# Performance work log

Hardware: AMD Instinct MI355X
Metric: run time of the kernel (lower is better)

Reference implementation:

```python
import jax, jax.numpy as jnp
import numpy as np

B, N, D, NUM_CLASSES = 2048, 32768, 256, 100

def setup_inputs() -> dict:
    key = jax.random.key(0)
    k1, k2, k3 = jax.random.split(key, 3)
    x = jax.random.normal(k1, (B, D), dtype=jnp.float32)
    support_embeddings = jax.random.normal(k2, (N, D), dtype=jnp.float32)
    support_labels = jax.random.randint(k3, (N,), 0, NUM_CLASSES, dtype=jnp.int64)
    return {
        "x": x,
        "support_embeddings": support_embeddings,
        "support_labels": support_labels,
        "num_classes": NUM_CLASSES,
    }

def reference(x, support_embeddings, support_labels, num_classes):
    # Pairwise L2 distance [B, N] via ||q||^2 + ||s||^2 - 2 q.s (avoids [B,N,D] broadcast)
    q2 = jnp.sum(x * x, axis=1, keepdims=True)                 # [B, 1]
    s2 = jnp.sum(support_embeddings * support_embeddings, axis=1)  # [N]
    cross = jnp.einsum('bd,nd->bn', x, support_embeddings)     # [B, N]
    dist = jnp.sqrt(jnp.maximum(q2 + s2[None, :] - 2.0 * cross, 0.0))
    # topk(-dist, k=1) over support axis -> nearest neighbor index
    _, idx = jax.lax.top_k(-dist, 1)                           # [B, 1]
    idx = jnp.squeeze(idx, axis=1)                             # [B]
    labels = jnp.take(support_labels, idx, axis=0)             # [B]
    one_hot = jax.nn.one_hot(labels, num_classes, dtype=jnp.int32)  # [B, num_classes]
    return one_hot
```

## Files before the change

### kernel.cpp

```cpp
#include <hip/hip_runtime.h>

#define BQ 2048
#define NS 32768
#define DIM 256
#define NROWS (NS + BQ)

#define BMQ 128
#define BNS 128
#define BK 32
#define NST (DIM / BK)
#define GY (NS / BNS)
#define EPS 0.08f
#define FBCH GY

typedef _Float16 f16;
typedef _Float16 f16x4 __attribute__((ext_vector_type(4)));
typedef _Float16 f16x8 __attribute__((ext_vector_type(8)));
typedef float    f32x4 __attribute__((ext_vector_type(4)));

__device__ __forceinline__ void gload16(const f16* g, f16* l) {
    __builtin_amdgcn_global_load_lds(
        (const __attribute__((address_space(1))) unsigned int*)g,
        (__attribute__((address_space(3))) unsigned int*)l, 16, 0, 0);
}

__device__ __forceinline__ const f16x8* fragp(const f16* base, int row, int q) {
    return (const f16x8*)(base + row * 32 + ((q ^ ((row >> 1) & 3)) << 3));
}

__global__ __launch_bounds__(256) void convert_kernel(
    const float* __restrict__ x, const float* __restrict__ sup,
    f16* __restrict__ xh, f16* __restrict__ sh,
    float* __restrict__ s2, int* __restrict__ fb_cnt) {
    if (blockIdx.x == 0 && threadIdx.x == 0) *fb_cnt = 0;
    const int wave = threadIdx.x >> 6, lane = threadIdx.x & 63;
    const int row = blockIdx.x * 4 + wave;
    if (row < NS) {
        float4 v = ((const float4*)(sup + (size_t)row * DIM))[lane];
        f16x4 hi;
        hi[0] = (f16)v.x; hi[1] = (f16)v.y; hi[2] = (f16)v.z; hi[3] = (f16)v.w;
        *(f16x4*)(sh + (size_t)row * DIM + lane * 4) = hi;
        float sum = v.x * v.x + v.y * v.y + v.z * v.z + v.w * v.w;
#pragma unroll
        for (int off = 32; off > 0; off >>= 1) sum += __shfl_xor(sum, off);
        if (lane == 0) s2[row] = sum;
    } else {
        const int q = row - NS;
        float4 v = ((const float4*)(x + (size_t)q * DIM))[lane];
        f16x4 hi;
        hi[0] = (f16)v.x; hi[1] = (f16)v.y; hi[2] = (f16)v.z; hi[3] = (f16)v.w;
        *(f16x4*)(xh + (size_t)q * DIM + lane * 4) = hi;
    }
}

__global__ __launch_bounds__(256) void knn_mfma(
    const f16* __restrict__ xh, const f16* __restrict__ sh,
    const float* __restrict__ s2g,
    float* __restrict__ pv1, float* __restrict__ pv2, int* __restrict__ pi1) {
    __shared__ f16 T[2][2][BMQ * 32];

    const int tid  = threadIdx.x;
    const int lane = tid & 63, wid = tid >> 6;
    const int l16  = lane & 15, quad = lane >> 4;
    const int m0   = blockIdx.x * BMQ;
    const int n0   = blockIdx.y * BNS;

    const int rl = lane >> 2;
    const int qs = (lane & 3) ^ ((rl >> 1) & 3);
    const size_t srcoff = (size_t)rl * DIM + qs * 8;

    const f16* px0 = xh + (size_t)(m0 + wid * 32) * DIM + srcoff;
    const f16* px1 = px0 + (size_t)16 * DIM;
    const f16* ps0 = sh + (size_t)(n0 + wid * 32) * DIM + srcoff;
    const f16* ps1 = ps0 + (size_t)16 * DIM;
    const int dX = wid * 1024;

    f32x4 acc[2][8];
#pragma unroll
    for (int fi = 0; fi < 2; ++fi)
#pragma unroll
        for (int fj = 0; fj < 8; ++fj) acc[fi][fj] = (f32x4){0.f, 0.f, 0.f, 0.f};

    gload16(px0, &T[0][0][dX]);
    gload16(px1, &T[0][0][dX + 512]);
    gload16(ps0, &T[0][1][dX]);
    gload16(ps1, &T[0][1][dX + 512]);

    for (int s = 0; s < NST; ++s) {
        __syncthreads();
        if (s + 1 < NST) {
            const int b = (s + 1) & 1, k0 = (s + 1) * BK;
            gload16(px0 + k0, &T[b][0][dX]);
            gload16(px1 + k0, &T[b][0][dX + 512]);
            gload16(ps0 + k0, &T[b][1][dX]);
            gload16(ps1 + k0, &T[b][1][dX + 512]);
        }
        const f16* TX = &T[s & 1][0][0];
        const f16* TS = &T[s & 1][1][0];

        f16x8 A0 = *fragp(TX, wid * 32 + l16,      quad);
        f16x8 A1 = *fragp(TX, wid * 32 + 16 + l16, quad);
#pragma unroll
        for (int fj = 0; fj < 8; ++fj) {
            f16x8 B = *fragp(TS, fj * 16 + l16, quad);
            acc[0][fj] = __builtin_amdgcn_mfma_f32_16x16x32_f16(A0, B, acc[0][fj], 0, 0, 0);
            acc[1][fj] = __builtin_amdgcn_mfma_f32_16x16x32_f16(A1, B, acc[1][fj], 0, 0, 0);
        }
    }

    float s2v[8];
#pragma unroll
    for (int fj = 0; fj < 8; ++fj) s2v[fj] = s2g[n0 + fj * 16 + l16];
#pragma unroll
    for (int fi = 0; fi < 2; ++fi)
#pragma unroll
        for (int rg = 0; rg < 4; ++rg) {
            float bv1 = 3.4e38f, bv2 = 3.4e38f; int bi = 0;
#pragma unroll
            for (int fj = 0; fj < 8; ++fj) {
                float s = fmaf(-2.f, acc[fi][fj][rg], s2v[fj]);
                bv2 = fminf(bv2, fmaxf(bv1, s));
                bi  = (s < bv1) ? (n0 + fj * 16 + l16) : bi;
                bv1 = fminf(bv1, s);
            }
#pragma unroll
            for (int m = 1; m < 16; m <<= 1) {
                float ov1 = __shfl_xor(bv1, m);
                float ov2 = __shfl_xor(bv2, m);
                int   oi  = __shfl_xor(bi, m);
                float nb2 = fminf(fminf(bv2, ov2), fmaxf(bv1, ov1));
                bi  = (ov1 < bv1) ? oi : bi;
                bv1 = fminf(bv1, ov1);
                bv2 = nb2;
            }
            if (l16 == 0) {
                const int row = m0 + wid * 32 + fi * 16 + quad * 4 + rg;
                pv1[(size_t)row * GY + blockIdx.y] = bv1;
                pv2[(size_t)row * GY + blockIdx.y] = bv2;
                pi1[(size_t)row * GY + blockIdx.y] = bi;
            }
        }
}

__global__ __launch_bounds__(128) void finalize2(
    const float* __restrict__ pv1, const float* __restrict__ pv2,
    const int* __restrict__ pi1, const int* __restrict__ labels,
    const int* __restrict__ ncp, int* __restrict__ out,
    int* __restrict__ fb_cnt, int* __restrict__ fb_list,
    float* __restrict__ qbest) {
    const int q = blockIdx.x, tid = threadIdx.x;
    __shared__ int s_label;
    if (tid < 64) {
        float bv1 = 3.4e38f, bv2 = 3.4e38f; int bi = 0;
        for (int t = tid; t < GY; t += 64) {
            float ov1 = pv1[(size_t)q * GY + t];
            float ov2 = pv2[(size_t)q * GY + t];
            int   oi  = pi1[(size_t)q * GY + t];
            float nb2 = fminf(fminf(bv2, ov2), fmaxf(bv1, ov1));
            bi  = (ov1 < bv1) ? oi : bi;
            bv1 = fminf(bv1, ov1);
            bv2 = nb2;
        }
#pragma unroll
        for (int m = 1; m < 64; m <<= 1) {
            float ov1 = __shfl_xor(bv1, m);
            float ov2 = __shfl_xor(bv2, m);
            int   oi  = __shfl_xor(bi, m);
            float nb2 = fminf(fminf(bv2, ov2), fmaxf(bv1, ov1));
            bi  = (ov1 < bv1) ? oi : bi;
            bv1 = fminf(bv1, ov1);
            bv2 = nb2;
        }
        if (tid == 0) {
            qbest[q] = bv1;
            if (bv2 - bv1 <= EPS) {
                int slot = atomicAdd(fb_cnt, 1);
                fb_list[slot] = q;
            }
            bool is64 = true;
            for (int i = 1; i < 128; i += 2)
                if (labels[i] != 0) { is64 = false; break; }
            s_label = is64 ? labels[2 * bi] : labels[bi];
        }
    }
    __syncthreads();
    const int nc = ncp[0], lbl = s_label;
    for (int c = tid; c < nc; c += 128)
        out[q * nc + c] = (c == lbl) ? 1 : 0;
}

__global__ __launch_bounds__(256) void fallback_scan(
    const float* __restrict__ x, const float* __restrict__ sup,
    const float* __restrict__ s2, const int* __restrict__ fb_cnt,
    const int* __restrict__ fb_list, const float* __restrict__ qbest,
    const float* __restrict__ pv1,
    float* __restrict__ fb_v, int* __restrict__ fb_i) {
    const int nslots = *fb_cnt;
    const int chunk = blockIdx.x;
    const int tid = threadIdx.x, lane = tid & 63, w = tid >> 6;
    __shared__ float wv[4];
    __shared__ int   wi[4];
    for (int slot = blockIdx.y; slot < nslots; slot += gridDim.y) {
        const int q = fb_list[slot];
        if (pv1[(size_t)q * GY + chunk] > qbest[q] + EPS) {
            if (tid == 0) {
                fb_v[(size_t)q * FBCH + chunk] = 3.4e38f;
                fb_i[(size_t)q * FBCH + chunk] = 0x7fffffff;
            }
            __syncthreads();
            continue;
        }
        const float4 xv = ((const float4*)(x + (size_t)q * DIM))[lane];
        float best = 3.4e38f; int bi = 0x7fffffff;
        const int base = chunk * BNS + w * 32;
#pragma unroll 4
        for (int r = 0; r < 32; ++r) {
            const int n = base + r;
            float4 sv = ((const float4*)(sup + (size_t)n * DIM))[lane];
            float d = fmaf(sv.x, xv.x,
                      fmaf(sv.y, xv.y,
                      fmaf(sv.z, xv.z, sv.w * xv.w)));
#pragma unroll
            for (int m = 32; m > 0; m >>= 1) d += __shfl_xor(d, m);
            float sc = s2[n] - 2.f * d;
            if (sc < best) { best = sc; bi = n; }
        }
        if (lane == 0) { wv[w] = best; wi[w] = bi; }
        __syncthreads();
        if (tid == 0) {
            float bv = wv[0]; int bx = wi[0];
#pragma unroll
            for (int t = 1; t < 4; ++t)
                if (wv[t] < bv || (wv[t] == bv && wi[t] < bx)) { bv = wv[t]; bx = wi[t]; }
            fb_v[(size_t)q * FBCH + chunk] = bv;
            fb_i[(size_t)q * FBCH + chunk] = bx;
        }
        __syncthreads();
    }
}

__global__ __launch_bounds__(64) void fallback_merge(
    const int* __restrict__ fb_cnt, const int* __restrict__ fb_list,
    const float* __restrict__ fb_v, const int* __restrict__ fb_i,
    const int* __restrict__ labels, const int* __restrict__ ncp,
    int* __restrict__ out) {
    const int nslots = *fb_cnt;
    const int lane = threadIdx.x;
    for (int slot = blockIdx.x; slot < nslots; slot += gridDim.x) {
        const int q = fb_list[slot];
        float v = 3.4e38f; int ix = 0x7fffffff;
        for (int t = lane; t < FBCH; t += 64) {
            float ov = fb_v[(size_t)q * FBCH + t];
            int   oi = fb_i[(size_t)q * FBCH + t];
            if (ov < v || (ov == v && oi < ix)) { v = ov; ix = oi; }
        }
#pragma unroll
        for (int m = 1; m < 64; m <<= 1) {
            float ov = __shfl_xor(v, m);
            int   oi = __shfl_xor(ix, m);
            if (ov < v || (ov == v && oi < ix)) { v = ov; ix = oi; }
        }
        bool is64 = true;
        for (int i = 1; i < 128; i += 2)
            if (labels[i] != 0) { is64 = false; break; }
        const int lbl = is64 ? labels[2 * ix] : labels[ix];
        const int nc = ncp[0];
        for (int c = lane; c < nc; c += 64)
            out[q * nc + c] = (c == lbl) ? 1 : 0;
    }
}

#define SBM 128
#define SBN 128
#define SBK 16
#define SNT 4
#define SGY (NS / (SBN * SNT))
#define SLDT (SBM + 4)

__global__ __launch_bounds__(256) void s2_kernel(const float* __restrict__ s,
                                                 float* __restrict__ s2) {
    int wave = threadIdx.x >> 6, lane = threadIdx.x & 63;
    int row = blockIdx.x * 4 + wave;
    const float4* p = (const float4*)(s + (size_t)row * DIM);
    float4 v = p[lane];
    float sum = v.x * v.x + v.y * v.y + v.z * v.z + v.w * v.w;
#pragma unroll
    for (int off = 32; off > 0; off >>= 1) sum += __shfl_xor(sum, off);
    if (lane == 0) s2[row] = sum;
}

__global__ __launch_bounds__(256) void knn_f32(const float* __restrict__ x,
                                               const float* __restrict__ sup,
                                               const float* __restrict__ s2g,
                                               float* __restrict__ pvals,
                                               int* __restrict__ pidx) {
    __shared__ float Xs[SBK][SLDT];
    __shared__ float Bs[SBK][SLDT];
    const int tid = threadIdx.x;
    const int tx = tid & 15, ty = tid >> 4;
    const int m0 = blockIdx.x * SBM, by = blockIdx.y;
    const int srow = tid >> 2, skq = (tid & 3) * 4;
    float rmin[8]; int ridx[8];
#pragma unroll
    for (int i = 0; i < 8; ++i) { rmin[i] = 3.4e38f; ridx[i] = 0x7fffffff; }
    const float* xr0 = x + (size_t)(m0 + srow) * DIM + skq;
    const float* xr1 = x + (size_t)(m0 + 64 + srow) * DIM + skq;
    for (int nt = 0; nt < SNT; ++nt) {
        const int n0 = (by * SNT + nt) * SBN;
        const float* sr0 = sup + (size_t)(n0 + srow) * DIM + skq;
        const float* sr1 = sup + (size_t)(n0 + 64 + srow) * DIM + skq;
        float acc[8][8];
#pragma unroll
        for (int i = 0; i < 8; ++i)
#pragma unroll
            for (int j = 0; j < 8; ++j) acc[i][j] = 0.0f;
        for (int kt = 0; kt < DIM / SBK; ++kt) {
            const int k0 = kt * SBK;
            float4 xv0 = *(const float4*)(xr0 + k0);
            float4 xv1 = *(const float4*)(xr1 + k0);
            float4 sv0 = *(const float4*)(sr0 + k0);
            float4 sv1 = *(const float4*)(sr1 + k0);
            __syncthreads();
            Xs[skq + 0][srow] = xv0.x; Xs[skq + 1][srow] = xv0.y;
            Xs[skq + 2][srow] = xv0.z; Xs[skq + 3][srow] = xv0.w;
            Xs[skq + 0][64 + srow] = xv1.x; Xs[skq + 1][64 + srow] = xv1.y;
            Xs[skq + 2][64 + srow] = xv1.z; Xs[skq + 3][64 + srow] = xv1.w;
            Bs[skq + 0][srow] = sv0.x; Bs[skq + 1][srow] = sv0.y;
            Bs[skq + 2][srow] = sv0.z; Bs[skq + 3][srow] = sv0.w;
            Bs[skq + 0][64 + srow] = sv1.x; Bs[skq + 1][64 + srow] = sv1.y;
            Bs[skq + 2][64 + srow] = sv1.z; Bs[skq + 3][64 + srow] = sv1.w;
            __syncthreads();
#pragma unroll
            for (int k = 0; k < SBK; ++k) {
                float4 a0 = *(const float4*)&Xs[k][ty * 4];
                float4 a1 = *(const float4*)&Xs[k][64 + ty * 4];
                float4 b0 = *(const float4*)&Bs[k][tx * 4];
                float4 b1 = *(const float4*)&Bs[k][64 + tx * 4];
                float a[8] = {a0.x, a0.y, a0.z, a0.w, a1.x, a1.y, a1.z, a1.w};
                float b[8] = {b0.x, b0.y, b0.z, b0.w, b1.x, b1.y, b1.z, b1.w};
#pragma unroll
                for (int i = 0; i < 8; ++i)
#pragma unroll
                    for (int j = 0; j < 8; ++j)
                        acc[i][j] = fmaf(a[i], b[j], acc[i][j]);
            }
        }
        const int nb0 = n0 + tx * 4, nb1 = n0 + 64 + tx * 4;
        float4 s20 = *(const float4*)(s2g + nb0);
        float4 s21 = *(const float4*)(s2g + nb1);
        float s2a[8] = {s20.x, s20.y, s20.z, s20.w, s21.x, s21.y, s21.z, s21.w};
        int nca[8] = {nb0, nb0 + 1, nb0 + 2, nb0 + 3, nb1, nb1 + 1, nb1 + 2, nb1 + 3};
#pragma unroll
        for (int i = 0; i < 8; ++i)
#pragma unroll
            for (int j = 0; j < 8; ++j) {
                float sc = fmaf(-2.0f, acc[i][j], s2a[j]);
                if (sc < rmin[i] || (sc == rmin[i] && nca[j] < ridx[i])) {
                    rmin[i] = sc; ridx[i] = nca[j];
                }
            }
    }
    __syncthreads();
    float* redv = (float*)Xs;
    int* redi = (int*)Bs;
#pragma unroll
    for (int i = 0; i < 8; ++i) {
        int mrow = (i < 4) ? (ty * 4 + i) : (64 + ty * 4 + (i - 4));
        redv[mrow * 16 + tx] = rmin[i];
        redi[mrow * 16 + tx] = ridx[i];
    }
    __syncthreads();
    if (tid < SBM) {
        float best = redv[tid * 16];
        int bi = redi[tid * 16];
#pragma unroll
        for (int t = 1; t < 16; ++t) {
            float v = redv[tid * 16 + t];
            int ix = redi[tid * 16 + t];
            if (v < best || (v == best && ix < bi)) { best = v; bi = ix; }
        }
        pvals[(size_t)(m0 + tid) * SGY + by] = best;
        pidx[(size_t)(m0 + tid) * SGY + by] = bi;
    }
}

__global__ __launch_bounds__(64) void finalize_f32(const float* __restrict__ pvals,
                                                   const int* __restrict__ pidx,
                                                   const int* __restrict__ labels,
                                                   const int* __restrict__ ncp,
                                                   int* __restrict__ out) {
    const int b = blockIdx.x, lane = threadIdx.x;
    float v = pvals[(size_t)b * SGY + lane];
    int ix = pidx[(size_t)b * SGY + lane];
#pragma unroll
    for (int off = 32; off > 0; off >>= 1) {
        float ov = __shfl_xor(v, off);
        int oi = __shfl_xor(ix, off);
        if (ov < v || (ov == v && oi < ix)) { v = ov; ix = oi; }
    }
    bool is64 = true;
    for (int i = 1; i < 128; i += 2)
        if (labels[i] != 0) { is64 = false; break; }
    const int lbl = is64 ? labels[2 * ix] : labels[ix];
    const int nc = ncp[0];
    for (int c = lane; c < nc; c += 64)
        out[b * nc + c] = (c == lbl) ? 1 : 0;
}

extern "C" void kernel_launch(void* const* d_in, const int* in_sizes, int n_in,
                              void* d_out, int out_size, void* d_ws, size_t ws_size,
                              hipStream_t stream) {
    const float* x      = (const float*)d_in[0];
    const float* sup    = (const float*)d_in[1];
    const int*   labels = (const int*)d_in[2];
    const int*   ncp    = (const int*)d_in[3];
    int* out = (int*)d_out;

    char* p = (char*)d_ws;
    float* s2      = (float*)p;           p += (size_t)NS * 4;
    float* pv1     = (float*)p;           p += (size_t)BQ * GY * 4;
    float* pv2     = (float*)p;           p += (size_t)BQ * GY * 4;
    int*   pi1     = (int*)p;             p += (size_t)BQ * GY * 4;
    int*   fb_cnt  = (int*)p;             p += 256;
    int*   fb_list = (int*)p;             p += (size_t)BQ * 4;
    float* qbest   = (float*)p;           p += (size_t)BQ * 4;
    float* fb_v    = (float*)p;           p += (size_t)BQ * FBCH * 4;
    int*   fb_i    = (int*)p;             p += (size_t)BQ * FBCH * 4;
    f16*   xh      = (f16*)p;             p += (size_t)BQ * DIM * 2;
    f16*   sh      = (f16*)p;             p += (size_t)NS * DIM * 2;
    const size_t need = (size_t)(p - (char*)d_ws);

    if (ws_size >= need) {
        convert_kernel<<<NROWS / 4, 256, 0, stream>>>(x, sup, xh, sh, s2, fb_cnt);
        dim3 grid(BQ / BMQ, GY);
        knn_mfma<<<grid, 256, 0, stream>>>(xh, sh, s2, pv1, pv2, pi1);
        finalize2<<<BQ, 128, 0, stream>>>(pv1, pv2, pi1, labels, ncp, out,
                                          fb_cnt, fb_list, qbest);
        dim3 fbgrid(FBCH, 64);
        fallback_scan<<<fbgrid, 256, 0, stream>>>(x, sup, s2, fb_cnt, fb_list,
                                                  qbest, pv1, fb_v, fb_i);
        fallback_merge<<<64, 64, 0, stream>>>(fb_cnt, fb_list, fb_v, fb_i, labels, ncp, out);
    } else {
        float* ss2   = (float*)d_ws;
        float* pvals = ss2 + NS;
        int*   pidx  = (int*)(pvals + (size_t)BQ * SGY);
        s2_kernel<<<NS / 4, 256, 0, stream>>>(sup, ss2);
        dim3 grid(BQ / SBM, SGY);
        knn_f32<<<grid, 256, 0, stream>>>(x, sup, ss2, pvals, pidx);
        finalize_f32<<<BQ, 64, 0, stream>>>(pvals, pidx, labels, ncp, out);
    }
}
```

Before: 158.9 us.

## Fuse finalize, fallback scan and merge into one per-query kernel

Three kernels (finalize2, fallback_scan, fallback_merge) become one per-query kernel with 256 threads, one per chunk partial. Each block reduces its query's top-2 partials and, only when the margin is ambiguous, rescans in fp32 just the candidate chunks within EPS of the best, entirely in-block. This removes two launches, the global fallback list, the atomic counter and the fb_v/fb_i scratch buffers. The cost is that ambiguous queries are rescanned serially by one block instead of across a 256-chunk grid, which could add a long tail if a query has many candidates.

```diff
diff --git a/kernel.cpp b/kernel.cpp
--- a/kernel.cpp
+++ b/kernel.cpp
@@ -11,7 +11,6 @@
 #define NST (DIM / BK)
 #define GY (NS / BNS)
 #define EPS 0.08f
-#define FBCH GY
 
 typedef _Float16 f16;
 typedef _Float16 f16x4 __attribute__((ext_vector_type(4)));
@@ -30,9 +29,7 @@
 
 __global__ __launch_bounds__(256) void convert_kernel(
     const float* __restrict__ x, const float* __restrict__ sup,
-    f16* __restrict__ xh, f16* __restrict__ sh,
-    float* __restrict__ s2, int* __restrict__ fb_cnt) {
-    if (blockIdx.x == 0 && threadIdx.x == 0) *fb_cnt = 0;
+    f16* __restrict__ xh, f16* __restrict__ sh, float* __restrict__ s2) {
     const int wave = threadIdx.x >> 6, lane = threadIdx.x & 63;
     const int row = blockIdx.x * 4 + wave;
     if (row < NS) {
@@ -142,77 +139,79 @@
         }
 }
 
-__global__ __launch_bounds__(128) void finalize2(
+__global__ __launch_bounds__(256) void finalize_fused(
     const float* __restrict__ pv1, const float* __restrict__ pv2,
-    const int* __restrict__ pi1, const int* __restrict__ labels,
-    const int* __restrict__ ncp, int* __restrict__ out,
-    int* __restrict__ fb_cnt, int* __restrict__ fb_list,
-    float* __restrict__ qbest) {
+    const int* __restrict__ pi1,
+    const float* __restrict__ x, const float* __restrict__ sup,
+    const float* __restrict__ s2, const int* __restrict__ labels,
+    const int* __restrict__ ncp, int* __restrict__ out) {
     const int q = blockIdx.x, tid = threadIdx.x;
-    __shared__ int s_label;
-    if (tid < 64) {
-        float bv1 = 3.4e38f, bv2 = 3.4e38f; int bi = 0;
-        for (int t = tid; t < GY; t += 64) {
-            float ov1 = pv1[(size_t)q * GY + t];
-            float ov2 = pv2[(size_t)q * GY + t];
-            int   oi  = pi1[(size_t)q * GY + t];
-            float nb2 = fminf(fminf(bv2, ov2), fmaxf(bv1, ov1));
-            bi  = (ov1 < bv1) ? oi : bi;
-            bv1 = fminf(bv1, ov1);
-            bv2 = nb2;
-        }
-#pragma unroll
-        for (int m = 1; m < 64; m <<= 1) {
-            float ov1 = __shfl_xor(bv1, m);
-            float ov2 = __shfl_xor(bv2, m);
-            int   oi  = __shfl_xor(bi, m);
-            float nb2 = fminf(fminf(bv2, ov2), fmaxf(bv1, ov1));
-            bi  = (ov1 < bv1) ? oi : bi;
-            bv1 = fminf(bv1, ov1);
-            bv2 = nb2;
-        }
-        if (tid == 0) {
-            qbest[q] = bv1;
-            if (bv2 - bv1 <= EPS) {
-                int slot = atomicAdd(fb_cnt, 1);
-                fb_list[slot] = q;
-            }
-            bool is64 = true;
-            for (int i = 1; i < 128; i += 2)
-                if (labels[i] != 0) { is64 = false; break; }
-            s_label = is64 ? labels[2 * bi] : labels[bi];
-        }
-    }
-    __syncthreads();
-    const int nc = ncp[0], lbl = s_label;
-    for (int c = tid; c < nc; c += 128)
-        out[q * nc + c] = (c == lbl) ? 1 : 0;
-}
-
-__global__ __launch_bounds__(256) void fallback_scan(
-    const float* __restrict__ x, const float* __restrict__ sup,
-    const float* __restrict__ s2, const int* __restrict__ fb_cnt,
-    const int* __restrict__ fb_list, const float* __restrict__ qbest,
-    const float* __restrict__ pv1,
-    float* __restrict__ fb_v, int* __restrict__ fb_i) {
-    const int nslots = *fb_cnt;
-    const int chunk = blockIdx.x;
-    const int tid = threadIdx.x, lane = tid & 63, w = tid >> 6;
-    __shared__ float wv[4];
-    __shared__ int   wi[4];
-    for (int slot = blockIdx.y; slot < nslots; slot += gridDim.y) {
-        const int q = fb_list[slot];
-        if (pv1[(size_t)q * GY + chunk] > qbest[q] + EPS) {
-            if (tid == 0) {
-                fb_v[(size_t)q * FBCH + chunk] = 3.4e38f;
-                fb_i[(size_t)q * FBCH + chunk] = 0x7fffffff;
-            }
-            __syncthreads();
-            continue;
-        }
-        const float4 xv = ((const float4*)(x + (size_t)q * DIM))[lane];
-        float best = 3.4e38f; int bi = 0x7fffffff;
-        const int base = chunk * BNS + w * 32;
+    const int lane = tid & 63, w = tid >> 6;
+    __shared__ float sv1[4], sv2[4];
+    __shared__ int   si[4];
+    __shared__ float s_bv1, s_bv2;
+    __shared__ int   s_bi, s_is64, s_label;
+    __shared__ int   cand[GY];
+    __shared__ int   ncand;
+    __shared__ float fwv[4];
+    __shared__ int   fwi[4];
+
+    float bv1 = pv1[(size_t)q * GY + tid];
+    float bv2 = pv2[(size_t)q * GY + tid];
+    int   bi  = pi1[(size_t)q * GY + tid];
+    const float myv1 = bv1;
+#pragma unroll
+    for (int m = 1; m < 64; m <<= 1) {
+        float ov1 = __shfl_xor(bv1, m);
+        float ov2 = __shfl_xor(bv2, m);
+        int   oi  = __shfl_xor(bi, m);
+        float nb2 = fminf(fminf(bv2, ov2), fmaxf(bv1, ov1));
+        bi  = (ov1 < bv1) ? oi : bi;
+        bv1 = fminf(bv1, ov1);
+        bv2 = nb2;
+    }
+    if (lane == 0) { sv1[w] = bv1; sv2[w] = bv2; si[w] = bi; }
+    if (w == 0) {
+        unsigned long long ball = __ballot(labels[2 * lane + 1] == 0);
+        if (lane == 0) s_is64 = (ball == ~0ULL) ? 1 : 0;
+    }
+    if (tid == 0) ncand = 0;
+    __syncthreads();
+    if (tid == 0) {
+        float fb1 = sv1[0], fb2 = sv2[0]; int fbi = si[0];
+#pragma unroll
+        for (int t = 1; t < 4; ++t) {
+            float nb2 = fminf(fminf(fb2, sv2[t]), fmaxf(fb1, sv1[t]));
+            fbi = (sv1[t] < fb1) ? si[t] : fbi;
+            fb1 = fminf(fb1, sv1[t]);
+            fb2 = nb2;
+        }
+        s_bv1 = fb1; s_bv2 = fb2; s_bi = fbi;
+    }
+    __syncthreads();
+
+    const int nc = ncp[0];
+    if (s_bv2 - s_bv1 > EPS) {
+        if (tid == 0)
+            s_label = s_is64 ? labels[2 * s_bi] : labels[s_bi];
+        __syncthreads();
+        const int lbl = s_label;
+        for (int c = tid; c < nc; c += 256)
+            out[q * nc + c] = (c == lbl) ? 1 : 0;
+        return;
+    }
+
+    if (myv1 <= s_bv1 + EPS) {
+        int slot = atomicAdd(&ncand, 1);
+        cand[slot] = tid;
+    }
+    __syncthreads();
+    const int ncd = ncand;
+    float best = 3.4e38f; int bix = 0x7fffffff;
+    for (int ci = 0; ci < ncd; ++ci) {
+        const int base = cand[ci] * BNS + w * 32;
+        const float4* xp = (const float4*)(x + (size_t)q * DIM);
+        const float4 xv = xp[lane];
 #pragma unroll 4
         for (int r = 0; r < 32; ++r) {
             const int n = base + r;
@@ -223,51 +222,22 @@
 #pragma unroll
             for (int m = 32; m > 0; m >>= 1) d += __shfl_xor(d, m);
             float sc = s2[n] - 2.f * d;
-            if (sc < best) { best = sc; bi = n; }
-        }
-        if (lane == 0) { wv[w] = best; wi[w] = bi; }
-        __syncthreads();
-        if (tid == 0) {
-            float bv = wv[0]; int bx = wi[0];
-#pragma unroll
-            for (int t = 1; t < 4; ++t)
-                if (wv[t] < bv || (wv[t] == bv && wi[t] < bx)) { bv = wv[t]; bx = wi[t]; }
-            fb_v[(size_t)q * FBCH + chunk] = bv;
-            fb_i[(size_t)q * FBCH + chunk] = bx;
-        }
-        __syncthreads();
-    }
-}
-
-__global__ __launch_bounds__(64) void fallback_merge(
-    const int* __restrict__ fb_cnt, const int* __restrict__ fb_list,
-    const float* __restrict__ fb_v, const int* __restrict__ fb_i,
-    const int* __restrict__ labels, const int* __restrict__ ncp,
-    int* __restrict__ out) {
-    const int nslots = *fb_cnt;
-    const int lane = threadIdx.x;
-    for (int slot = blockIdx.x; slot < nslots; slot += gridDim.x) {
-        const int q = fb_list[slot];
-        float v = 3.4e38f; int ix = 0x7fffffff;
-        for (int t = lane; t < FBCH; t += 64) {
-            float ov = fb_v[(size_t)q * FBCH + t];
-            int   oi = fb_i[(size_t)q * FBCH + t];
-            if (ov < v || (ov == v && oi < ix)) { v = ov; ix = oi; }
-        }
-#pragma unroll
-        for (int m = 1; m < 64; m <<= 1) {
-            float ov = __shfl_xor(v, m);
-            int   oi = __shfl_xor(ix, m);
-            if (ov < v || (ov == v && oi < ix)) { v = ov; ix = oi; }
-        }
-        bool is64 = true;
-        for (int i = 1; i < 128; i += 2)
-            if (labels[i] != 0) { is64 = false; break; }
-        const int lbl = is64 ? labels[2 * ix] : labels[ix];
-        const int nc = ncp[0];
-        for (int c = lane; c < nc; c += 64)
-            out[q * nc + c] = (c == lbl) ? 1 : 0;
-    }
+            if (sc < best || (sc == best && n < bix)) { best = sc; bix = n; }
+        }
+    }
+    if (lane == 0) { fwv[w] = best; fwi[w] = bix; }
+    __syncthreads();
+    if (tid == 0) {
+        float fb = fwv[0]; int fx = fwi[0];
+#pragma unroll
+        for (int t = 1; t < 4; ++t)
+            if (fwv[t] < fb || (fwv[t] == fb && fwi[t] < fx)) { fb = fwv[t]; fx = fwi[t]; }
+        s_label = s_is64 ? labels[2 * fx] : labels[fx];
+    }
+    __syncthreads();
+    const int lbl = s_label;
+    for (int c = tid; c < nc; c += 256)
+        out[q * nc + c] = (c == lbl) ? 1 : 0;
 }
 
 #define SBM 128
@@ -417,36 +387,27 @@
     int* out = (int*)d_out;
 
     char* p = (char*)d_ws;
-    float* s2      = (float*)p;           p += (size_t)NS * 4;
-    float* pv1     = (float*)p;           p += (size_t)BQ * GY * 4;
-    float* pv2     = (float*)p;           p += (size_t)BQ * GY * 4;
-    int*   pi1     = (int*)p;             p += (size_t)BQ * GY * 4;
-    int*   fb_cnt  = (int*)p;             p += 256;
-    int*   fb_list = (int*)p;             p += (size_t)BQ * 4;
-    float* qbest   = (float*)p;           p += (size_t)BQ * 4;
-    float* fb_v    = (float*)p;           p += (size_t)BQ * FBCH * 4;
-    int*   fb_i    = (int*)p;             p += (size_t)BQ * FBCH * 4;
-    f16*   xh      = (f16*)p;             p += (size_t)BQ * DIM * 2;
-    f16*   sh      = (f16*)p;             p += (size_t)NS * DIM * 2;
+    float* s2  = (float*)p;               p += (size_t)NS * 4;
+    float* pv1 = (float*)p;               p += (size_t)BQ * GY * 4;
+    float* pv2 = (float*)p;               p += (size_t)BQ * GY * 4;
+    int*   pi1 = (int*)p;                 p += (size_t)BQ * GY * 4;
+    f16*   xh  = (f16*)p;                 p += (size_t)BQ * DIM * 2;
+    f16*   sh  = (f16*)p;                 p += (size_t)NS * DIM * 2;
     const size_t need = (size_t)(p - (char*)d_ws);
 
     if (ws_size >= need) {
-        convert_kernel<<<NROWS / 4, 256, 0, stream>>>(x, sup, xh, sh, s2, fb_cnt);
+        convert_kernel<<<NROWS / 4, 256, 0, stream>>>(x, sup, xh, sh, s2);
         dim3 grid(BQ / BMQ, GY);
         knn_mfma<<<grid, 256, 0, stream>>>(xh, sh, s2, pv1, pv2, pi1);
-        finalize2<<<BQ, 128, 0, stream>>>(pv1, pv2, pi1, labels, ncp, out,
-                                          fb_cnt, fb_list, qbest);
-        dim3 fbgrid(FBCH, 64);
-        fallback_scan<<<fbgrid, 256, 0, stream>>>(x, sup, s2, fb_cnt, fb_list,
-                                                  qbest, pv1, fb_v, fb_i);
-        fallback_merge<<<64, 64, 0, stream>>>(fb_cnt, fb_list, fb_v, fb_i, labels, ncp, out);
+        finalize_fused<<<BQ, 256, 0, stream>>>(pv1, pv2, pi1, x, sup, s2,
+                                               labels, ncp, out);
     } else {
         float* ss2   = (float*)d_ws;
         float* pvals = ss2 + NS;
         int*   pidx  = (int*)(pvals + (size_t)BQ * SGY);
         s2_kernel<<<NS / 4, 256, 0, stream>>>(sup, ss2);
-        dim3 grid(BQ / SBM, SGY);
-        knn_f32<<<grid, 256, 0, stream>>>(x, sup, ss2, pvals, pidx);
+        dim3 sgrid(BQ / SBM, SGY);
+        knn_f32<<<sgrid, 256, 0, stream>>>(x, sup, ss2, pvals, pidx);
         finalize_f32<<<BQ, 64, 0, stream>>>(pvals, pidx, labels, ncp, out);
     }
 }
```

Measured after the change: 189.0 us. 18.9% more time.
